# Optimization experiments

Hardware: AMD Instinct MI355X
Metric: run time of the kernel (lower is better)

## Reference

```python
import jax, jax.numpy as jnp
import numpy as np

N_NODES = 100000
N_EDGES = 1600000
N_CLASS = 26
HIDDEN = 128


def gcn_conv(x, W, b, row, col, ew, n):
    """PyG GCNConv with normalize=True, add_self_loops=True (fill 1.0).

    row/col/ew already include self-loops. x: [N, Fin], W: [Fin, Fout].
    """
    deg = jax.ops.segment_sum(ew, col, num_segments=n)            # [N]
    dis = jnp.where(deg > 0, jax.lax.rsqrt(jnp.maximum(deg, 1e-30)), 0.0)
    norm = dis[row] * ew * dis[col]                               # [E+N]
    h = x @ W                                                     # [N, Fout]
    msg = h[row] * norm[:, None]                                  # gather + scale
    out = jax.ops.segment_sum(msg, col, num_segments=n)           # scatter-add
    return out + b


def setup_inputs() -> dict:
    key = jax.random.key(0)
    k1, k2, k3, k4, k5, k6, k7, k8, k9 = jax.random.split(key, 9)
    x = jax.random.normal(k1, (N_NODES, N_CLASS), dtype=jnp.float32)
    edge_index = jax.random.randint(k2, (2, N_EDGES), 0, N_NODES, dtype=jnp.int64)
    edge_weight = jax.random.uniform(k3, (N_EDGES,), dtype=jnp.float32)
    s1 = 1.0 / np.sqrt(N_CLASS)
    s2 = 1.0 / np.sqrt(HIDDEN)
    W1 = jax.random.uniform(k4, (N_CLASS, HIDDEN), jnp.float32, -s1, s1)
    b1 = jnp.zeros((HIDDEN,), jnp.float32)
    W2 = jax.random.uniform(k5, (HIDDEN, HIDDEN), jnp.float32, -s2, s2)
    b2 = jnp.zeros((HIDDEN,), jnp.float32)
    Wfc = jax.random.uniform(k6, (HIDDEN, N_CLASS), jnp.float32, -s2, s2)
    bfc = jax.random.uniform(k7, (N_CLASS,), jnp.float32, -s2, s2)
    return {"x": x, "edge_index": edge_index, "edge_weight": edge_weight,
            "W1": W1, "b1": b1, "W2": W2, "b2": b2, "Wfc": Wfc, "bfc": bfc}


def reference(x, edge_index, edge_weight, W1, b1, W2, b2, Wfc, bfc):
    n = x.shape[0]
    loop = jnp.arange(n, dtype=edge_index.dtype)
    row = jnp.concatenate([edge_index[0], loop])   # sources (with self-loops)
    col = jnp.concatenate([edge_index[1], loop])   # targets
    ew = jnp.concatenate([edge_weight, jnp.ones((n,), edge_weight.dtype)])
    h = jax.nn.relu(gcn_conv(x, W1, b1, row, col, ew, n))
    h = jax.nn.relu(gcn_conv(h, W2, b2, row, col, ew, n))
    return h @ Wfc + bfc
```

## Files before the change

### kernel.cpp

```cpp
#include <hip/hip_runtime.h>
#include <hip/hip_fp16.h>

#define N_NODES 100000
#define N_EDGES 1600000
#define HIDDEN  128
#define N_CLASS 26

#define BUK_SHIFT 9
#define BUK_DSTS  512
#define NBUK      196
#define BUK_CAP   10240
#define PB_EDGES  8192
#define PB_BLOCKS ((N_EDGES + PB_EDGES - 1) / PB_EDGES)

typedef _Float16 f16x2 __attribute__((ext_vector_type(2)));

__device__ __forceinline__ float fdot2(__half2 a, __half2 b, float c) {
#if __has_builtin(__builtin_amdgcn_fdot2)
    union { __half2 h; f16x2 v; } ua, ub;
    ua.h = a; ub.h = b;
    return __builtin_amdgcn_fdot2(ua.v, ub.v, c, false);
#else
    float2 fa = __half22float2(a), fb = __half22float2(b);
    return c + fa.x * fb.x + fa.y * fb.y;
#endif
}

union U4 { uint4 u; __half2 h[4]; };
union U2 { uint2 u; __half2 h[2]; };
union UW { int i; __half2 h; };


__global__ __launch_bounds__(1024) void bucket_kernel(const int* __restrict__ row,
                                                      const int* __restrict__ col,
                                                      const float* __restrict__ ew,
                                                      int* __restrict__ bukcnt,
                                                      int2* __restrict__ stage) {
    __shared__ int2 outst[PB_EDGES];
    __shared__ unsigned short bukof[PB_EDGES];
    __shared__ int cnt[NBUK], ofs[NBUK], cur[NBUK], gt[NBUK];
    __shared__ int sc[256];
    const int tid = threadIdx.x;
    const int e0 = blockIdx.x * PB_EDGES;
    const int nvalid = min(PB_EDGES, N_EDGES - e0);

    for (int b = tid; b < NBUK; b += 1024) { cnt[b] = 0; cur[b] = 0; }
    __syncthreads();

    int mykey[8]; float myw[8]; int mybuk[8];
#pragma unroll
    for (int i = 0; i < 8; ++i) {
        int idx = tid + i * 1024;
        mybuk[i] = -1;
        if (idx < nvalid) {
            int e = e0 + idx;
            int d = col[e], r = row[e];
            int buk = d >> BUK_SHIFT;
            mykey[i] = ((d & (BUK_DSTS - 1)) << 17) | r;
            myw[i] = ew[e];
            mybuk[i] = buk;
            atomicAdd(&cnt[buk], 1);
        }
    }
    __syncthreads();

    {
        int c = (tid < NBUK) ? cnt[tid] : 0;
        if (tid < 256) sc[tid] = c;
        __syncthreads();
        for (int o = 1; o < 256; o <<= 1) {
            int v = 0;
            if (tid < 256 && tid >= o) v = sc[tid - o];
            __syncthreads();
            if (tid < 256) sc[tid] += v;
            __syncthreads();
        }
        if (tid < NBUK) ofs[tid] = sc[tid] - c;
        __syncthreads();
    }

#pragma unroll
    for (int i = 0; i < 8; ++i) {
        if (mybuk[i] >= 0) {
            int s = ofs[mybuk[i]] + atomicAdd(&cur[mybuk[i]], 1);
            outst[s] = make_int2(mykey[i], __float_as_int(myw[i]));
            bukof[s] = (unsigned short)mybuk[i];
        }
    }
    __syncthreads();

    if (tid < NBUK) {
        int c = cnt[tid];
        int gb = (c > 0) ? atomicAdd(&bukcnt[tid], c) : 0;
        gt[tid] = tid * BUK_CAP + gb;
    }
    __syncthreads();

    for (int i = tid; i < nvalid; i += 1024) {
        int b = bukof[i];
        stage[(size_t)gt[b] + (i - ofs[b])] = outst[i];
    }
}


__global__ void bukscan_kernel(const int* __restrict__ bukcnt, int* __restrict__ bukbase,
                               int* __restrict__ start) {
    __shared__ int s[256];
    int tid = threadIdx.x;
    int c = (tid < NBUK) ? bukcnt[tid] : 0;
    s[tid] = c;
    __syncthreads();
    for (int o = 1; o < 256; o <<= 1) {
        int v = (tid >= o) ? s[tid - o] : 0;
        __syncthreads();
        s[tid] += v;
        __syncthreads();
    }
    if (tid < NBUK) bukbase[tid] = s[tid] - c;
    if (tid == 0) start[N_NODES] = N_EDGES;
}


__global__ __launch_bounds__(1024) void csr_kernel(const int2* __restrict__ stage,
                                                   const int* __restrict__ bukcnt,
                                                   const int* __restrict__ bukbase,
                                                   const float* __restrict__ x,
                                                   int* __restrict__ start,
                                                   float* __restrict__ dinv,
                                                   __half* __restrict__ x16,
                                                   int2* __restrict__ packed) {
    __shared__ unsigned int cnt5[BUK_DSTS];
    __shared__ int ofs5[BUK_DSTS];
    __shared__ unsigned int cur5[BUK_DSTS];
    __shared__ float deg5[BUK_DSTS];
    __shared__ float dv5[BUK_DSTS];
    __shared__ int sc[BUK_DSTS];
    const int tid = threadIdx.x;
    const int b = blockIdx.x;
    const int total = bukcnt[b];
    const int base = bukbase[b];
    const int2* st = stage + (size_t)b * BUK_CAP;

    for (int j = tid; j < BUK_DSTS; j += 1024) { cnt5[j] = 0; cur5[j] = 0; deg5[j] = 0.0f; }
    __syncthreads();

    for (int i = tid; i < total; i += 1024) {
        int2 en = st[i];
        int dl = en.x >> 17;
        atomicAdd(&cnt5[dl], 1u);
        atomicAdd(&deg5[dl], __int_as_float(en.y));
    }
    __syncthreads();

    {
        int c = (tid < BUK_DSTS) ? (int)cnt5[tid] : 0;
        if (tid < BUK_DSTS) sc[tid] = c;
        __syncthreads();
        for (int o = 1; o < BUK_DSTS; o <<= 1) {
            int v = 0;
            if (tid < BUK_DSTS && tid >= o) v = sc[tid - o];
            __syncthreads();
            if (tid < BUK_DSTS) sc[tid] += v;
            __syncthreads();
        }
        if (tid < BUK_DSTS) ofs5[tid] = sc[tid] - c;
        __syncthreads();
    }

    if (tid < BUK_DSTS) {
        int d = (b << BUK_SHIFT) + tid;
        if (d < N_NODES) {
            float dv = rsqrtf(deg5[tid] + 1.0f);
            dv5[tid] = dv;
            dinv[d] = dv;
            start[d] = base + ofs5[tid];
        }
    }
    __syncthreads();

    for (int t = tid; t < BUK_DSTS * 32; t += 1024) {
        int j = t >> 5, l = t & 31;
        int d = (b << BUK_SHIFT) + j;
        if (d < N_NODES) {
            float v = (l < N_CLASS) ? x[(size_t)d * N_CLASS + l] * dv5[j] : 0.0f;
            x16[((size_t)d << 5) + l] = __float2half(v);
        }
    }

    for (int i = tid; i < total; i += 1024) {
        int2 en = st[i];
        int dl = en.x >> 17;
        int src = en.x & 0x1FFFF;
        unsigned int r = atomicAdd(&cur5[dl], 1u);
        unsigned int hw = __half_as_ushort(__float2half(__int_as_float(en.y)));
        packed[(size_t)base + ofs5[dl] + (int)r] = make_int2(src, (int)(hw | (hw << 16)));
    }
}


__global__ __launch_bounds__(256) void gather26_kernel(const __half* __restrict__ x16,
                                                       const int* __restrict__ start,
                                                       const int2* __restrict__ packed,
                                                       const float* __restrict__ dinv,
                                                       float* __restrict__ aggx) {
    const int g = blockIdx.x * 32 + (threadIdx.x >> 3);
    const int l = threadIdx.x & 7;
    const uint2* X = reinterpret_cast<const uint2*>(x16);
    U2 sv; sv.u = X[((size_t)g << 3) + l];
    __half2 acc0 = sv.h[0], acc1 = sv.h[1];
    int s = start[g], t = start[g + 1];
    int i = s;
    for (; i + 4 <= t; i += 4) {
        int2 p0 = packed[i], p1 = packed[i + 1], p2 = packed[i + 2], p3 = packed[i + 3];
        U2 v0, v1, v2, v3;
        v0.u = X[((size_t)p0.x << 3) + l];
        v1.u = X[((size_t)p1.x << 3) + l];
        v2.u = X[((size_t)p2.x << 3) + l];
        v3.u = X[((size_t)p3.x << 3) + l];
        UW w0, w1, w2, w3;
        w0.i = p0.y; w1.i = p1.y; w2.i = p2.y; w3.i = p3.y;
        acc0 = __hfma2(w0.h, v0.h[0], acc0); acc1 = __hfma2(w0.h, v0.h[1], acc1);
        acc0 = __hfma2(w1.h, v1.h[0], acc0); acc1 = __hfma2(w1.h, v1.h[1], acc1);
        acc0 = __hfma2(w2.h, v2.h[0], acc0); acc1 = __hfma2(w2.h, v2.h[1], acc1);
        acc0 = __hfma2(w3.h, v3.h[0], acc0); acc1 = __hfma2(w3.h, v3.h[1], acc1);
    }
    for (; i < t; ++i) {
        int2 p = packed[i];
        U2 v; v.u = X[((size_t)p.x << 3) + l];
        UW w; w.i = p.y;
        acc0 = __hfma2(w.h, v.h[0], acc0); acc1 = __hfma2(w.h, v.h[1], acc1);
    }
    float dg = dinv[g];
    float2 a = __half22float2(acc0), b = __half22float2(acc1);
    float4 o = make_float4(dg * a.x, dg * a.y, dg * b.x, dg * b.y);
    reinterpret_cast<float4*>(aggx)[((size_t)g << 3) + l] = o;
}


__global__ __launch_bounds__(256) void gemmB_kernel(const float* __restrict__ aggx,
                                                    const float* __restrict__ W1,
                                                    const float* __restrict__ b1,
                                                    __half* __restrict__ h16) {
    __shared__ float axs[64][32];
    const int tid = threadIdx.x;
    const int nb = blockIdx.x * 64;
    for (int t = tid; t < 64 * 32 / 4; t += 256) {
        int node = nb + (t >> 3);
        reinterpret_cast<float4*>(axs)[t] =
            (node < N_NODES)
                ? reinterpret_cast<const float4*>(aggx)[((size_t)node << 3) + (t & 7)]
                : make_float4(0.f, 0.f, 0.f, 0.f);
    }
    const int c  = tid & 127;
    const int nr = tid >> 7;
    float w[N_CLASS];
#pragma unroll
    for (int k = 0; k < N_CLASS; ++k) w[k] = W1[k * HIDDEN + c];
    const float bias = b1[c];
    __syncthreads();
    for (int tt = 0; tt < 32; ++tt) {
        int n = nr + 2 * tt;
        int node = nb + n;
        if (node < N_NODES) {
            float acc = bias;
#pragma unroll
            for (int k = 0; k < N_CLASS; ++k) acc += axs[n][k] * w[k];
            h16[(size_t)node * HIDDEN + c] = __float2half(fmaxf(acc, 0.0f));
        }
    }
}


#define CB_NODES 128
__global__ __launch_bounds__(512) void gemmC_kernel(const __half* __restrict__ h16,
                                                    const float* __restrict__ W2,
                                                    const float* __restrict__ dinv,
                                                    __half* __restrict__ p16) {
    __shared__ __half2 hs2[CB_NODES][HIDDEN / 2];
    __shared__ __half2 ws2[HIDDEN / 2][HIDDEN];
    const int tid = threadIdx.x;
    const int nb = blockIdx.x * CB_NODES;
    for (int t = tid; t < HIDDEN / 2 * HIDDEN; t += 512) {
        int k2 = t >> 7, c = t & 127;
        ws2[k2][c] = __floats2half2_rn(W2[(2 * k2) * HIDDEN + c], W2[(2 * k2 + 1) * HIDDEN + c]);
    }
    for (int t = tid; t < CB_NODES * 16; t += 512) {
        int node = nb + (t >> 4);
        reinterpret_cast<uint4*>(hs2)[t] =
            (node < N_NODES)
                ? reinterpret_cast<const uint4*>(h16)[(size_t)node * 16 + (t & 15)]
                : make_uint4(0u, 0u, 0u, 0u);
    }
    __syncthreads();
    const int c4 = (tid & 31) * 4;
    const int n0 = (tid >> 5) * 8;
    float acc[8][4] = {};
    for (int k2 = 0; k2 < HIDDEN / 2; k2 += 2) {
        U4 wa, wb;
        wa.u = *reinterpret_cast<const uint4*>(&ws2[k2][c4]);
        wb.u = *reinterpret_cast<const uint4*>(&ws2[k2 + 1][c4]);
#pragma unroll
        for (int i = 0; i < 8; ++i) {
            U2 hv; hv.u = *reinterpret_cast<const uint2*>(&hs2[n0 + i][k2]);
#pragma unroll
            for (int q = 0; q < 4; ++q) {
                acc[i][q] = fdot2(hv.h[0], wa.h[q], acc[i][q]);
                acc[i][q] = fdot2(hv.h[1], wb.h[q], acc[i][q]);
            }
        }
    }
#pragma unroll
    for (int i = 0; i < 8; ++i) {
        int node = nb + n0 + i;
        if (node < N_NODES) {
            float d = dinv[node];
            union { __half2 h2[2]; uint2 u; } pk;
            pk.h2[0] = __floats2half2_rn(d * acc[i][0], d * acc[i][1]);
            pk.h2[1] = __floats2half2_rn(d * acc[i][2], d * acc[i][3]);
            *reinterpret_cast<uint2*>(&p16[(size_t)node * HIDDEN + c4]) = pk.u;
        }
    }
}


__global__ __launch_bounds__(256) void aggfc_kernel(const __half* __restrict__ p16,
                                                    const int* __restrict__ start,
                                                    const int2* __restrict__ packed,
                                                    const float* __restrict__ dinv,
                                                    const float* __restrict__ b2,
                                                    const float* __restrict__ Wfc,
                                                    const float* __restrict__ bfc,
                                                    float* __restrict__ out) {
    __shared__ __half2 wf2[HIDDEN / 2][N_CLASS];
    __shared__ float bfs[N_CLASS];
    __shared__ __half2 zs2[16][HIDDEN / 2];
    const int tid = threadIdx.x;
    for (int t = tid; t < HIDDEN / 2 * N_CLASS; t += 256) {
        int k2 = t / N_CLASS, j = t % N_CLASS;
        wf2[k2][j] = __floats2half2_rn(Wfc[(2 * k2) * N_CLASS + j], Wfc[(2 * k2 + 1) * N_CLASS + j]);
    }
    if (tid < N_CLASS) bfs[tid] = bfc[tid];
    __syncthreads();

    const int grp = tid >> 4;
    const int l   = tid & 15;
    const int g   = blockIdx.x * 16 + grp;
    const uint4* P = reinterpret_cast<const uint4*>(p16);

    U4 sv; sv.u = P[((size_t)g << 4) + l];
    __half2 acc0 = sv.h[0], acc1 = sv.h[1], acc2 = sv.h[2], acc3 = sv.h[3];

    int s = start[g], t = start[g + 1];
    int i = s;
    for (; i + 2 <= t; i += 2) {
        int2 pa = packed[i], pb = packed[i + 1];
        U4 va, vb;
        va.u = P[((size_t)pa.x << 4) + l];
        vb.u = P[((size_t)pb.x << 4) + l];
        UW wa, wb; wa.i = pa.y; wb.i = pb.y;
        acc0 = __hfma2(wa.h, va.h[0], acc0); acc1 = __hfma2(wa.h, va.h[1], acc1);
        acc2 = __hfma2(wa.h, va.h[2], acc2); acc3 = __hfma2(wa.h, va.h[3], acc3);
        acc0 = __hfma2(wb.h, vb.h[0], acc0); acc1 = __hfma2(wb.h, vb.h[1], acc1);
        acc2 = __hfma2(wb.h, vb.h[2], acc2); acc3 = __hfma2(wb.h, vb.h[3], acc3);
    }
    for (; i < t; ++i) {
        int2 p = packed[i];
        U4 v; v.u = P[((size_t)p.x << 4) + l];
        UW w; w.i = p.y;
        acc0 = __hfma2(w.h, v.h[0], acc0); acc1 = __hfma2(w.h, v.h[1], acc1);
        acc2 = __hfma2(w.h, v.h[2], acc2); acc3 = __hfma2(w.h, v.h[3], acc3);
    }

    const float dg = dinv[g];
    const int f = l * 8;
    float4 ba = *reinterpret_cast<const float4*>(&b2[f]);
    float4 bb = *reinterpret_cast<const float4*>(&b2[f + 4]);
    float2 f0 = __half22float2(acc0), f1 = __half22float2(acc1);
    float2 f2 = __half22float2(acc2), f3 = __half22float2(acc3);
    zs2[grp][l * 4 + 0] = __floats2half2_rn(fmaxf(dg * f0.x + ba.x, 0.f), fmaxf(dg * f0.y + ba.y, 0.f));
    zs2[grp][l * 4 + 1] = __floats2half2_rn(fmaxf(dg * f1.x + ba.z, 0.f), fmaxf(dg * f1.y + ba.w, 0.f));
    zs2[grp][l * 4 + 2] = __floats2half2_rn(fmaxf(dg * f2.x + bb.x, 0.f), fmaxf(dg * f2.y + bb.y, 0.f));
    zs2[grp][l * 4 + 3] = __floats2half2_rn(fmaxf(dg * f3.x + bb.z, 0.f), fmaxf(dg * f3.y + bb.w, 0.f));
#pragma unroll
    for (int jj = l; jj < N_CLASS; jj += 16) {
        float accf = bfs[jj];
#pragma unroll 16
        for (int k2 = 0; k2 < HIDDEN / 2; ++k2)
            accf = fdot2(zs2[grp][k2], wf2[k2][jj], accf);
        out[(size_t)g * N_CLASS + jj] = accf;
    }
}


extern "C" void kernel_launch(void* const* d_in, const int* in_sizes, int n_in,
                              void* d_out, int out_size, void* d_ws, size_t ws_size,
                              hipStream_t stream) {
    const float* x   = (const float*)d_in[0];
    const int*   ei  = (const int*)  d_in[1];
    const float* ew  = (const float*)d_in[2];
    const float* W1  = (const float*)d_in[3];
    const float* b1  = (const float*)d_in[4];
    const float* W2  = (const float*)d_in[5];
    const float* b2  = (const float*)d_in[6];
    const float* Wfc = (const float*)d_in[7];
    const float* bfc = (const float*)d_in[8];
    float* out = (float*)d_out;

    const int n = N_NODES, E = N_EDGES;
    const int* row = ei;
    const int* col = ei + E;

    char* ws = (char*)d_ws;
    size_t off = 0;
    auto alloc = [&](size_t bytes) -> void* {
        void* ptr = ws + off;
        off += (bytes + 255) & ~(size_t)255;
        return ptr;
    };
    int*   bukcnt  = (int*)  alloc(NBUK * 4);
    int*   bukbase = (int*)  alloc(NBUK * 4);
    float* dinv    = (float*)alloc((size_t)n * 4);
    int*   start   = (int*)  alloc((size_t)(n + 1) * 4);
    int2*  packed  = (int2*) alloc((size_t)E * 8);
    __half* x16    = (__half*)alloc((size_t)n * 32 * 2);
    float* aggx    = (float*)alloc((size_t)n * 32 * 4);
    __half* h16    = (__half*)alloc((size_t)n * HIDDEN * 2 < (size_t)NBUK * BUK_CAP * 8
                                        ? (size_t)NBUK * BUK_CAP * 8
                                        : (size_t)n * HIDDEN * 2);
    __half* p16    = (__half*)alloc((size_t)n * HIDDEN * 2);
    int2*  stage   = (int2*)h16;

    hipMemsetAsync(bukcnt, 0, NBUK * 4, stream);
    bucket_kernel<<<PB_BLOCKS, 1024, 0, stream>>>(row, col, ew, bukcnt, stage);
    bukscan_kernel<<<1, 256, 0, stream>>>(bukcnt, bukbase, start);
    csr_kernel<<<NBUK, 1024, 0, stream>>>(stage, bukcnt, bukbase, x, start, dinv, x16, packed);

    gather26_kernel<<<(n + 31) / 32, 256, 0, stream>>>(x16, start, packed, dinv, aggx);
    gemmB_kernel<<<(n + 63) / 64, 256, 0, stream>>>(aggx, W1, b1, h16);

    gemmC_kernel<<<(n + CB_NODES - 1) / CB_NODES, 512, 0, stream>>>(h16, W2, dinv, p16);
    aggfc_kernel<<<(n + 15) / 16, 256, 0, stream>>>(p16, start, packed, dinv, b2, Wfc, bfc, out);
}
```

Baseline: 228.8 us.

## Fuse layer-1 gather with GEMM and process nodes in degree-sorted order

Merges the 26-wide neighbor gather and the W1 projection into one kernel so aggregated features stay in shared memory, which removes the aggx round trip through global memory and one launch. The CSR kernel now counting-sorts each 512-node bucket by in-degree into a permutation. Both gather kernels walk nodes through this permutation so the nodes sharing a wavefront have similar edge counts, reducing divergence. It also unrolls the layer-2 edge loop by four and pads a shared array to avoid bank conflicts, at the cost of scattered output writes and extra work in the CSR kernel.

```diff
diff --git a/kernel.cpp b/kernel.cpp
--- a/kernel.cpp
+++ b/kernel.cpp
@@ -128,13 +128,16 @@
                                                    int* __restrict__ start,
                                                    float* __restrict__ dinv,
                                                    __half* __restrict__ x16,
-                                                   int2* __restrict__ packed) {
+                                                   int2* __restrict__ packed,
+                                                   int* __restrict__ perm) {
     __shared__ unsigned int cnt5[BUK_DSTS];
     __shared__ int ofs5[BUK_DSTS];
     __shared__ unsigned int cur5[BUK_DSTS];
     __shared__ float deg5[BUK_DSTS];
     __shared__ float dv5[BUK_DSTS];
     __shared__ int sc[BUK_DSTS];
+    __shared__ int dhist[128];
+    __shared__ int dcur[128];
     const int tid = threadIdx.x;
     const int b = blockIdx.x;
     const int total = bukcnt[b];
@@ -142,6 +145,7 @@
     const int2* st = stage + (size_t)b * BUK_CAP;
 
     for (int j = tid; j < BUK_DSTS; j += 1024) { cnt5[j] = 0; cur5[j] = 0; deg5[j] = 0.0f; }
+    if (tid < 128) { dhist[tid] = 0; dcur[tid] = 0; }
     __syncthreads();
 
     for (int i = tid; i < total; i += 1024) {
@@ -165,6 +169,15 @@
         }
         if (tid < BUK_DSTS) ofs5[tid] = sc[tid] - c;
         __syncthreads();
+    }
+
+    int myd = -1;
+    {
+        int d = (b << BUK_SHIFT) + tid;
+        if (tid < BUK_DSTS && d < N_NODES) {
+            myd = min((int)cnt5[tid], 127);
+            atomicAdd(&dhist[myd], 1);
+        }
     }
 
     if (tid < BUK_DSTS) {
@@ -178,6 +191,20 @@
     }
     __syncthreads();
 
+    if (tid < 128) sc[tid] = dhist[tid];
+    __syncthreads();
+    for (int o = 1; o < 128; o <<= 1) {
+        int v = 0;
+        if (tid < 128 && tid >= o) v = sc[tid - o];
+        __syncthreads();
+        if (tid < 128) sc[tid] += v;
+        __syncthreads();
+    }
+    if (myd >= 0) {
+        int rank = sc[myd] - dhist[myd] + atomicAdd(&dcur[myd], 1);
+        perm[(b << BUK_SHIFT) + rank] = (b << BUK_SHIFT) + tid;
+    }
+
     for (int t = tid; t < BUK_DSTS * 32; t += 1024) {
         int j = t >> 5, l = t & 31;
         int d = (b << BUK_SHIFT) + j;
@@ -198,75 +225,67 @@
 }
 
 
-__global__ __launch_bounds__(256) void gather26_kernel(const __half* __restrict__ x16,
-                                                       const int* __restrict__ start,
-                                                       const int2* __restrict__ packed,
-                                                       const float* __restrict__ dinv,
-                                                       float* __restrict__ aggx) {
-    const int g = blockIdx.x * 32 + (threadIdx.x >> 3);
-    const int l = threadIdx.x & 7;
-    const uint2* X = reinterpret_cast<const uint2*>(x16);
-    U2 sv; sv.u = X[((size_t)g << 3) + l];
-    __half2 acc0 = sv.h[0], acc1 = sv.h[1];
-    int s = start[g], t = start[g + 1];
-    int i = s;
-    for (; i + 4 <= t; i += 4) {
-        int2 p0 = packed[i], p1 = packed[i + 1], p2 = packed[i + 2], p3 = packed[i + 3];
-        U2 v0, v1, v2, v3;
-        v0.u = X[((size_t)p0.x << 3) + l];
-        v1.u = X[((size_t)p1.x << 3) + l];
-        v2.u = X[((size_t)p2.x << 3) + l];
-        v3.u = X[((size_t)p3.x << 3) + l];
-        UW w0, w1, w2, w3;
-        w0.i = p0.y; w1.i = p1.y; w2.i = p2.y; w3.i = p3.y;
-        acc0 = __hfma2(w0.h, v0.h[0], acc0); acc1 = __hfma2(w0.h, v0.h[1], acc1);
-        acc0 = __hfma2(w1.h, v1.h[0], acc0); acc1 = __hfma2(w1.h, v1.h[1], acc1);
-        acc0 = __hfma2(w2.h, v2.h[0], acc0); acc1 = __hfma2(w2.h, v2.h[1], acc1);
-        acc0 = __hfma2(w3.h, v3.h[0], acc0); acc1 = __hfma2(w3.h, v3.h[1], acc1);
-    }
-    for (; i < t; ++i) {
-        int2 p = packed[i];
-        U2 v; v.u = X[((size_t)p.x << 3) + l];
-        UW w; w.i = p.y;
-        acc0 = __hfma2(w.h, v.h[0], acc0); acc1 = __hfma2(w.h, v.h[1], acc1);
-    }
-    float dg = dinv[g];
-    float2 a = __half22float2(acc0), b = __half22float2(acc1);
-    float4 o = make_float4(dg * a.x, dg * a.y, dg * b.x, dg * b.y);
-    reinterpret_cast<float4*>(aggx)[((size_t)g << 3) + l] = o;
-}
-
-
-__global__ __launch_bounds__(256) void gemmB_kernel(const float* __restrict__ aggx,
-                                                    const float* __restrict__ W1,
-                                                    const float* __restrict__ b1,
-                                                    __half* __restrict__ h16) {
-    __shared__ float axs[64][32];
+__global__ __launch_bounds__(256) void layer1_kernel(const __half* __restrict__ x16,
+                                                     const int* __restrict__ start,
+                                                     const int2* __restrict__ packed,
+                                                     const float* __restrict__ dinv,
+                                                     const int* __restrict__ perm,
+                                                     const float* __restrict__ W1,
+                                                     const float* __restrict__ b1,
+                                                     __half* __restrict__ h16) {
+    __shared__ float axs[32][32];
+    __shared__ int gl[32];
     const int tid = threadIdx.x;
-    const int nb = blockIdx.x * 64;
-    for (int t = tid; t < 64 * 32 / 4; t += 256) {
-        int node = nb + (t >> 3);
-        reinterpret_cast<float4*>(axs)[t] =
-            (node < N_NODES)
-                ? reinterpret_cast<const float4*>(aggx)[((size_t)node << 3) + (t & 7)]
-                : make_float4(0.f, 0.f, 0.f, 0.f);
-    }
-    const int c  = tid & 127;
-    const int nr = tid >> 7;
+    const int nb = blockIdx.x * 32;
+    {
+        const int j = tid >> 3;
+        const int l = tid & 7;
+        const int g = perm[nb + j];
+        if (l == 0) gl[j] = g;
+        const uint2* X = reinterpret_cast<const uint2*>(x16);
+        U2 sv; sv.u = X[((size_t)g << 3) + l];
+        __half2 acc0 = sv.h[0], acc1 = sv.h[1];
+        int s = start[g], t = start[g + 1];
+        int i = s;
+        for (; i + 4 <= t; i += 4) {
+            int2 p0 = packed[i], p1 = packed[i + 1], p2 = packed[i + 2], p3 = packed[i + 3];
+            U2 v0, v1, v2, v3;
+            v0.u = X[((size_t)p0.x << 3) + l];
+            v1.u = X[((size_t)p1.x << 3) + l];
+            v2.u = X[((size_t)p2.x << 3) + l];
+            v3.u = X[((size_t)p3.x << 3) + l];
+            UW w0, w1, w2, w3;
+            w0.i = p0.y; w1.i = p1.y; w2.i = p2.y; w3.i = p3.y;
+            acc0 = __hfma2(w0.h, v0.h[0], acc0); acc1 = __hfma2(w0.h, v0.h[1], acc1);
+            acc0 = __hfma2(w1.h, v1.h[0], acc0); acc1 = __hfma2(w1.h, v1.h[1], acc1);
+            acc0 = __hfma2(w2.h, v2.h[0], acc0); acc1 = __hfma2(w2.h, v2.h[1], acc1);
+            acc0 = __hfma2(w3.h, v3.h[0], acc0); acc1 = __hfma2(w3.h, v3.h[1], acc1);
+        }
+        for (; i < t; ++i) {
+            int2 p = packed[i];
+            U2 v; v.u = X[((size_t)p.x << 3) + l];
+            UW w; w.i = p.y;
+            acc0 = __hfma2(w.h, v.h[0], acc0); acc1 = __hfma2(w.h, v.h[1], acc1);
+        }
+        float dg = dinv[g];
+        float2 a = __half22float2(acc0), bb = __half22float2(acc1);
+        *reinterpret_cast<float4*>(&axs[j][l * 4]) =
+            make_float4(dg * a.x, dg * a.y, dg * bb.x, dg * bb.y);
+    }
+    __syncthreads();
+    const int c = tid & 127;
+    const int half = tid >> 7;
     float w[N_CLASS];
 #pragma unroll
     for (int k = 0; k < N_CLASS; ++k) w[k] = W1[k * HIDDEN + c];
     const float bias = b1[c];
-    __syncthreads();
-    for (int tt = 0; tt < 32; ++tt) {
-        int n = nr + 2 * tt;
-        int node = nb + n;
-        if (node < N_NODES) {
-            float acc = bias;
-#pragma unroll
-            for (int k = 0; k < N_CLASS; ++k) acc += axs[n][k] * w[k];
-            h16[(size_t)node * HIDDEN + c] = __float2half(fmaxf(acc, 0.0f));
-        }
+#pragma unroll
+    for (int tt = 0; tt < 16; ++tt) {
+        int n = half + 2 * tt;
+        float acc = bias;
+#pragma unroll
+        for (int k = 0; k < N_CLASS; ++k) acc += axs[n][k] * w[k];
+        h16[(size_t)gl[n] * HIDDEN + c] = __float2half(fmaxf(acc, 0.0f));
     }
 }
 
@@ -327,13 +346,14 @@
                                                     const int* __restrict__ start,
                                                     const int2* __restrict__ packed,
                                                     const float* __restrict__ dinv,
+                                                    const int* __restrict__ perm,
                                                     const float* __restrict__ b2,
                                                     const float* __restrict__ Wfc,
                                                     const float* __restrict__ bfc,
                                                     float* __restrict__ out) {
     __shared__ __half2 wf2[HIDDEN / 2][N_CLASS];
     __shared__ float bfs[N_CLASS];
-    __shared__ __half2 zs2[16][HIDDEN / 2];
+    __shared__ __half2 zs2[16][65];
     const int tid = threadIdx.x;
     for (int t = tid; t < HIDDEN / 2 * N_CLASS; t += 256) {
         int k2 = t / N_CLASS, j = t % N_CLASS;
@@ -344,7 +364,7 @@
 
     const int grp = tid >> 4;
     const int l   = tid & 15;
-    const int g   = blockIdx.x * 16 + grp;
+    const int g   = perm[blockIdx.x * 16 + grp];
     const uint4* P = reinterpret_cast<const uint4*>(p16);
 
     U4 sv; sv.u = P[((size_t)g << 4) + l];
@@ -352,16 +372,22 @@
 
     int s = start[g], t = start[g + 1];
     int i = s;
-    for (; i + 2 <= t; i += 2) {
-        int2 pa = packed[i], pb = packed[i + 1];
-        U4 va, vb;
+    for (; i + 4 <= t; i += 4) {
+        int2 pa = packed[i], pb = packed[i + 1], pc = packed[i + 2], pd = packed[i + 3];
+        U4 va, vb, vc, vd;
         va.u = P[((size_t)pa.x << 4) + l];
         vb.u = P[((size_t)pb.x << 4) + l];
-        UW wa, wb; wa.i = pa.y; wb.i = pb.y;
+        vc.u = P[((size_t)pc.x << 4) + l];
+        vd.u = P[((size_t)pd.x << 4) + l];
+        UW wa, wb, wc, wd; wa.i = pa.y; wb.i = pb.y; wc.i = pc.y; wd.i = pd.y;
         acc0 = __hfma2(wa.h, va.h[0], acc0); acc1 = __hfma2(wa.h, va.h[1], acc1);
         acc2 = __hfma2(wa.h, va.h[2], acc2); acc3 = __hfma2(wa.h, va.h[3], acc3);
         acc0 = __hfma2(wb.h, vb.h[0], acc0); acc1 = __hfma2(wb.h, vb.h[1], acc1);
         acc2 = __hfma2(wb.h, vb.h[2], acc2); acc3 = __hfma2(wb.h, vb.h[3], acc3);
+        acc0 = __hfma2(wc.h, vc.h[0], acc0); acc1 = __hfma2(wc.h, vc.h[1], acc1);
+        acc2 = __hfma2(wc.h, vc.h[2], acc2); acc3 = __hfma2(wc.h, vc.h[3], acc3);
+        acc0 = __hfma2(wd.h, vd.h[0], acc0); acc1 = __hfma2(wd.h, vd.h[1], acc1);
+        acc2 = __hfma2(wd.h, vd.h[2], acc2); acc3 = __hfma2(wd.h, vd.h[3], acc3);
     }
     for (; i < t; ++i) {
         int2 p = packed[i];
@@ -421,9 +447,9 @@
     int*   bukbase = (int*)  alloc(NBUK * 4);
     float* dinv    = (float*)alloc((size_t)n * 4);
     int*   start   = (int*)  alloc((size_t)(n + 1) * 4);
+    int*   perm    = (int*)  alloc((size_t)n * 4);
     int2*  packed  = (int2*) alloc((size_t)E * 8);
     __half* x16    = (__half*)alloc((size_t)n * 32 * 2);
-    float* aggx    = (float*)alloc((size_t)n * 32 * 4);
     __half* h16    = (__half*)alloc((size_t)n * HIDDEN * 2 < (size_t)NBUK * BUK_CAP * 8
                                         ? (size_t)NBUK * BUK_CAP * 8
                                         : (size_t)n * HIDDEN * 2);
@@ -433,11 +459,10 @@
     hipMemsetAsync(bukcnt, 0, NBUK * 4, stream);
     bucket_kernel<<<PB_BLOCKS, 1024, 0, stream>>>(row, col, ew, bukcnt, stage);
     bukscan_kernel<<<1, 256, 0, stream>>>(bukcnt, bukbase, start);
-    csr_kernel<<<NBUK, 1024, 0, stream>>>(stage, bukcnt, bukbase, x, start, dinv, x16, packed);
-
-    gather26_kernel<<<(n + 31) / 32, 256, 0, stream>>>(x16, start, packed, dinv, aggx);
-    gemmB_kernel<<<(n + 63) / 64, 256, 0, stream>>>(aggx, W1, b1, h16);
+    csr_kernel<<<NBUK, 1024, 0, stream>>>(stage, bukcnt, bukbase, x, start, dinv, x16, packed, perm);
+
+    layer1_kernel<<<(n + 31) / 32, 256, 0, stream>>>(x16, start, packed, dinv, perm, W1, b1, h16);
 
     gemmC_kernel<<<(n + CB_NODES - 1) / CB_NODES, 512, 0, stream>>>(h16, W2, dinv, p16);
-    aggfc_kernel<<<(n + 15) / 16, 256, 0, stream>>>(p16, start, packed, dinv, b2, Wfc, bfc, out);
-}
+    aggfc_kernel<<<(n + 15) / 16, 256, 0, stream>>>(p16, start, packed, dinv, perm, b2, Wfc, bfc, out);
+}
```

Measured after the change: 221.2 us. 3.3% less time.
